# Kernel optimization log

Hardware: AMD Instinct MI355X
Metric: run time of the kernel (lower is better)

The kernel has to match this reference:

```python
import jax, jax.numpy as jnp
import numpy as np

# ---- constants from init_kwargs ----
LAM = 0.05      # lam_l2
CG_MAX = 10     # cg_max
B, C, H, W = 8, 12, 384, 384
EPS = 1e-12


def _cplx(a):
    # [..., 2] real/imag -> complex
    return jax.lax.complex(a[..., 0], a[..., 1])


def _ri(z):
    return jnp.stack([jnp.real(z), jnp.imag(z)], axis=-1)


def setup_inputs() -> dict:
    key = jax.random.key(0)
    k1, k2, k3, k4 = jax.random.split(key, 4)
    x = jax.random.normal(k1, (B, H, W, 2), dtype=jnp.float32)
    adj = jax.random.normal(k2, (B, H, W, 2), dtype=jnp.float32)  # A^H b
    maps = jax.random.normal(k3, (B, C, H, W, 2), dtype=jnp.float32) / np.sqrt(C).astype(np.float32)
    mask = (jax.random.uniform(k4, (B, H, W)) < 0.4).astype(jnp.float32)
    return {"x": x, "adj": adj, "maps": maps, "mask": mask}


def reference(x, adj, maps, mask):
    xc = _cplx(x)          # [B,H,W] complex image (network estimate)
    adjc = _cplx(adj)      # [B,H,W] A^H b
    mc = _cplx(maps)       # [B,C,H,W] coil sensitivities
    maskc = mask.astype(jnp.complex64)[:, None]  # [B,1,H,W]

    def normal(v):
        # SENSE normal operator: A^H A v
        cim = mc * v[:, None]                               # [B,C,H,W]
        k = jnp.fft.fft2(cim, norm="ortho")
        im = jnp.fft.ifft2(k * maskc, norm="ortho")
        return jnp.sum(jnp.conj(mc) * im, axis=1)           # [B,H,W]

    def Aop(v):
        # (A^H A + lam I) v
        return normal(v) + LAM * v

    def zdot(a, b):
        # per-batch real inner product Re<a,b>
        return jnp.real(jnp.sum(jnp.conj(a) * b, axis=(1, 2)))[:, None, None]

    # rhs = adj + lam * x ; CG initialized at rhs (flare.ConjGrad.forward(rhs))
    rhs = adjc + LAM * xc
    x0 = rhs
    r = rhs - Aop(x0)
    p = r
    rd = zdot(r, r)

    def step(carry, _):
        xk, r, p, rd = carry
        Ap = Aop(p)
        alpha = rd / (zdot(p, Ap) + EPS)
        xk = xk + alpha * p
        r = r - alpha * Ap
        rd_new = zdot(r, r)
        beta = rd_new / (rd + EPS)
        p = r + beta * p
        return (xk, r, p, rd_new), None

    (xk, _, _, _), _ = jax.lax.scan(step, (x0, r, p, rd), None, length=CG_MAX)
    return _ri(xk)  # [B,H,W,2]
```

## Files before the change

### kernel.cpp

```cpp
#include <hip/hip_runtime.h>
#include <math.h>

#define BB 8
#define CC 12
#define HH 384
#define WW 384
#define NPIX (HH*WW)
#define LAMF 0.05f
#define EPSF 1e-12f
#define NITER 10

typedef float2 c2;

__device__ __forceinline__ c2 mkc(float x, float y){ c2 r; r.x=x; r.y=y; return r; }
__device__ __forceinline__ c2 cadd(c2 a, c2 b){ return mkc(a.x+b.x, a.y+b.y); }
__device__ __forceinline__ c2 csub(c2 a, c2 b){ return mkc(a.x-b.x, a.y-b.y); }
__device__ __forceinline__ c2 cmul(c2 a, c2 b){ return mkc(a.x*b.x - a.y*b.y, a.x*b.y + a.y*b.x); }
__device__ __forceinline__ c2 cmulcj(c2 a, c2 b){ return mkc(a.x*b.x + a.y*b.y, a.x*b.y - a.y*b.x); }
__device__ __forceinline__ c2 cax(float s, c2 a, c2 b){ return mkc(fmaf(s,a.x,b.x), fmaf(s,a.y,b.y)); }
__device__ __forceinline__ c2 rot90(c2 a, float d){ return mkc(d*a.y, -d*a.x); }

template<int DIR> __device__ __forceinline__ void dft3(c2&a0,c2&a1,c2&a2){
  const float d=(float)DIR;
  c2 t=cadd(a1,a2), s=csub(a1,a2);
  c2 m=mkc(a0.x-0.5f*t.x, a0.y-0.5f*t.y);
  const float c=0.8660254037844386f*d;
  c2 w=mkc(c*s.y, -c*s.x);
  a0=cadd(a0,t); a1=cadd(m,w); a2=csub(m,w);
}
template<int DIR> __device__ __forceinline__ void dft6(c2 u[6]){
  c2 e0=u[0],e1=u[2],e2=u[4], o0=u[1],o1=u[3],o2=u[5];
  dft3<DIR>(e0,e1,e2); dft3<DIR>(o0,o1,o2);
  const float d=(float)DIR, q=0.8660254037844386f*d;
  c2 w1=mkc(0.5f,-q), w2=mkc(-0.5f,-q);
  c2 b1=cmul(w1,o1), b2=cmul(w2,o2);
  u[0]=cadd(e0,o0); u[3]=csub(e0,o0);
  u[1]=cadd(e1,b1); u[4]=csub(e1,b1);
  u[2]=cadd(e2,b2); u[5]=csub(e2,b2);
}
template<int DIR> __device__ __forceinline__ void dft8(c2 u[8]){
  const float d=(float)DIR;
  c2 t0=cadd(u[0],u[4]), t1=csub(u[0],u[4]);
  c2 t2=cadd(u[2],u[6]), t3=csub(u[2],u[6]);
  c2 E0=cadd(t0,t2), E2=csub(t0,t2);
  c2 r3=rot90(t3,d);
  c2 E1=cadd(t1,r3), E3=csub(t1,r3);
  c2 s0=cadd(u[1],u[5]), s1=csub(u[1],u[5]);
  c2 s2=cadd(u[3],u[7]), s3=csub(u[3],u[7]);
  c2 O0=cadd(s0,s2), O2v=csub(s0,s2);
  c2 r7=rot90(s3,d);
  c2 O1=cadd(s1,r7), O3=csub(s1,r7);
  const float rs=0.7071067811865476f;
  c2 w81=mkc(rs,-rs*d), w83=mkc(-rs,-rs*d);
  O1=cmul(w81,O1); O2v=rot90(O2v,d); O3=cmul(w83,O3);
  u[0]=cadd(E0,O0); u[4]=csub(E0,O0);
  u[1]=cadd(E1,O1); u[5]=csub(E1,O1);
  u[2]=cadd(E2,O2v); u[6]=csub(E2,O2v);
  u[3]=cadd(E3,O3); u[7]=csub(E3,O3);
}

__device__ __forceinline__ int pidx(int i){ return i + (i/48); }

__device__ __forceinline__ void make_tw(int t, c2 tw2[7], c2 tw3[7]){
  const float TP = 6.28318530717958647692f;
  int k2 = t % 6;
  #pragma unroll
  for (int j=1;j<8;j++){
    float s,c;
    sincosf(-TP*(float)(k2*j)*(1.0f/48.0f), &s, &c);
    tw2[j-1]=mkc(c,s);
    sincosf(-TP*(float)(t*j)*(1.0f/384.0f), &s, &c);
    tw3[j-1]=mkc(c,s);
  }
}

template<int DIR>
__device__ __forceinline__ void fft384(c2 u6[6], c2 o8[8], c2* SA, c2* SB,
                                       int t, const c2 tw2[7], const c2 tw3[7])
{
  dft6<DIR>(u6);
  #pragma unroll
  for (int j=0;j<6;j++) SA[pidx(6*t+j)] = u6[j];
  __syncthreads();
  if (t<48){
    c2 u[8];
    #pragma unroll
    for (int j=0;j<8;j++) u[j]=SA[pidx(t+48*j)];
    #pragma unroll
    for (int j=1;j<8;j++){
      c2 w=tw2[j-1]; if (DIR<0) w.y=-w.y;
      u[j]=cmul(u[j],w);
    }
    dft8<DIR>(u);
    int k=t%6; int base=(t-k)*8+k;
    #pragma unroll
    for (int j=0;j<8;j++) SB[pidx(base+6*j)]=u[j];
  }
  __syncthreads();
  if (t<48){
    c2 u[8];
    #pragma unroll
    for (int j=0;j<8;j++) u[j]=SB[pidx(t+48*j)];
    #pragma unroll
    for (int j=1;j<8;j++){
      c2 w=tw3[j-1]; if (DIR<0) w.y=-w.y;
      u[j]=cmul(u[j],w);
    }
    dft8<DIR>(u);
    #pragma unroll
    for (int j=0;j<8;j++) o8[j]=u[j];
  }
}

template<int MODE>
__global__ __launch_bounds__(256)
void k1_fwd(const c2* __restrict__ xin, const c2* __restrict__ adj,
            const c2* __restrict__ maps, c2* __restrict__ WK,
            const c2* __restrict__ rbuf, const c2* __restrict__ pin,
            c2* __restrict__ pout, const float* __restrict__ bNum,
            const float* __restrict__ bDen)
{
  __shared__ c2 tile[16][387];
  __shared__ c2 scratch[4][2][392];
  const int tid=threadIdx.x, t=tid&63, wv=tid>>6;
  const int NT=HH/16;
  int bid=blockIdx.x;
  int ht=bid%NT, c=(bid/NT)%CC, b=bid/(NT*CC);
  int h0=ht*16;
  c2 tw2[7], tw3[7]; make_tw(t,tw2,tw3);
  float beta=0.f;
  if (MODE==1) beta = bNum[b]/(bDen[b]+EPSF);
  c2* SA=scratch[wv][0];
  c2* SB=scratch[wv][1];
  const c2* mb = maps + (size_t)(b*CC+c)*NPIX;
  for (int i=0;i<4;i++){
    int rr=wv*4+i, h=h0+rr;
    size_t ro=((size_t)b*HH+h)*WW;
    const c2* mrow=mb+(size_t)h*WW;
    c2 u6[6];
    #pragma unroll
    for (int j=0;j<6;j++){
      int w=t+64*j;
      c2 v;
      if (MODE==0){
        v = cax(LAMF, xin[ro+w], adj[ro+w]);
      } else {
        v = cax(beta, pin[ro+w], rbuf[ro+w]);
        if (c==0) pout[ro+w]=v;
      }
      u6[j]=cmul(mrow[w], v);
    }
    c2 o8[8];
    fft384<1>(u6,o8,SA,SB,t,tw2,tw3);
    if (t<48){
      #pragma unroll
      for (int j=0;j<8;j++) tile[rr][t+48*j]=o8[j];
    }
  }
  __syncthreads();
  c2* wkc = WK + (size_t)(b*CC+c)*NPIX;
  int rl=tid&15, wg=tid>>4;
  for (int it=0;it<24;it++){
    int w=it*16+wg;
    wkc[(size_t)w*HH + h0 + rl] = tile[rl][w];
  }
}

__global__ __launch_bounds__(256)
void k2_mid(c2* __restrict__ WK, const float* __restrict__ maskT)
{
  __shared__ c2 scratch[4][2][392];
  const int tid=threadIdx.x, t=tid&63, wv=tid>>6;
  const int NT=WW/16;
  int bid=blockIdx.x;
  int wt=bid%NT, c=(bid/NT)%CC, b=bid/(NT*CC);
  c2 tw2[7], tw3[7]; make_tw(t,tw2,tw3);
  c2* SA=scratch[wv][0]; c2* SB=scratch[wv][1];
  for (int i=0;i<4;i++){
    int w=wt*16+wv*4+i;
    c2* row = WK + ((size_t)(b*CC+c)*WW + w)*HH;
    const float* mrow = maskT + ((size_t)b*WW + w)*HH;
    c2 u6[6];
    #pragma unroll
    for (int j=0;j<6;j++) u6[j]=row[t+64*j];
    c2 o8[8];
    fft384<1>(u6,o8,SA,SB,t,tw2,tw3);
    __syncthreads();
    if (t<48){
      #pragma unroll
      for (int j=0;j<8;j++){
        float m=mrow[t+48*j];
        c2 v=o8[j];
        SB[t+48*j]=mkc(v.x*m, v.y*m);
      }
    }
    __syncthreads();
    #pragma unroll
    for (int j=0;j<6;j++) u6[j]=SB[t+64*j];
    __syncthreads();
    c2 o8b[8];
    fft384<-1>(u6,o8b,SA,SB,t,tw2,tw3);
    if (t<48){
      #pragma unroll
      for (int j=0;j<8;j++) row[t+48*j]=o8b[j];
    }
  }
}

template<int MODE>
__global__ __launch_bounds__(256)
void k3_inv(const c2* __restrict__ WK, const c2* __restrict__ maps,
            const c2* __restrict__ xin, const c2* __restrict__ adj,
            const c2* __restrict__ pin, c2* __restrict__ rbuf,
            c2* __restrict__ Apbuf, c2* __restrict__ xout,
            float* __restrict__ accslot)
{
  __shared__ c2 tile[8][387];
  __shared__ c2 scratch[4][2][392];
  const int tid=threadIdx.x, t=tid&63, wv=tid>>6;
  const int NT=HH/8;
  int bid=blockIdx.x;
  int ht=bid%NT, b=bid/NT;
  int h0=ht*8;
  c2 tw2[7],tw3[7]; make_tw(t,tw2,tw3);
  c2* SA=scratch[wv][0]; c2* SB=scratch[wv][1];
  c2 acc[2][8];
  #pragma unroll
  for(int a=0;a<2;a++){
    #pragma unroll
    for(int q=0;q<8;q++) acc[a][q]=mkc(0.f,0.f);
  }
  int jj=tid&7, wq=tid>>3;
  for (int c=0;c<CC;c++){
    const c2* wkc = WK + (size_t)(b*CC+c)*NPIX;
    __syncthreads();
    for (int it=0;it<12;it++){
      int w=it*32+wq;
      tile[jj][w]=wkc[(size_t)w*HH + h0 + jj];
    }
    __syncthreads();
    const c2* mb = maps + (size_t)(b*CC+c)*NPIX;
    #pragma unroll
    for (int rl=0;rl<2;rl++){
      int j=wv*2+rl, h=h0+j;
      c2 u6[6];
      #pragma unroll
      for (int q=0;q<6;q++) u6[q]=tile[j][t+64*q];
      c2 o8[8];
      fft384<-1>(u6,o8,SA,SB,t,tw2,tw3);
      if (t<48){
        const c2* mrow=mb+(size_t)h*WW;
        #pragma unroll
        for (int q=0;q<8;q++){
          acc[rl][q]=cadd(acc[rl][q], cmulcj(mrow[t+48*q], o8[q]));
        }
      }
    }
  }
  float partial=0.f;
  #pragma unroll
  for (int rl=0;rl<2;rl++){
    int h=h0+wv*2+rl;
    size_t ro=((size_t)b*HH+h)*WW;
    if (t<48){
      #pragma unroll
      for (int q=0;q<8;q++){
        int w=t+48*q;
        if (MODE==0){
          c2 rhs = cax(LAMF, xin[ro+w], adj[ro+w]);
          c2 Ap = cax(LAMF, rhs, acc[rl][q]);
          c2 rv = csub(rhs, Ap);
          rbuf[ro+w]=rv;
          xout[ro+w]=rhs;
          partial = fmaf(rv.x,rv.x,fmaf(rv.y,rv.y,partial));
        } else {
          c2 pv = pin[ro+w];
          c2 Ap = cax(LAMF, pv, acc[rl][q]);
          Apbuf[ro+w]=Ap;
          partial = fmaf(pv.x,Ap.x,fmaf(pv.y,Ap.y,partial));
        }
      }
    }
  }
  #pragma unroll
  for (int o=32;o>0;o>>=1) partial += __shfl_down(partial,o);
  if (t==0) atomicAdd(&accslot[b], partial);
}

__global__ __launch_bounds__(256)
void k4_upd(c2* __restrict__ x, c2* __restrict__ rbuf,
            const c2* __restrict__ p, const c2* __restrict__ Ap,
            const float* __restrict__ rdPrev, const float* __restrict__ pApk,
            float* __restrict__ rdNew)
{
  const int PERB = NPIX/1024;
  int bid=blockIdx.x;
  int b=bid/PERB, blk=bid%PERB;
  float alpha = rdPrev[b]/(pApk[b]+EPSF);
  size_t base=(size_t)b*NPIX + (size_t)blk*1024 + threadIdx.x;
  float partial=0.f;
  #pragma unroll
  for (int i=0;i<4;i++){
    size_t idx=base + i*256;
    c2 pv=p[idx], apv=Ap[idx], xv=x[idx], rv=rbuf[idx];
    xv = cax(alpha, pv, xv);
    rv = cax(-alpha, apv, rv);
    x[idx]=xv; rbuf[idx]=rv;
    partial = fmaf(rv.x,rv.x,fmaf(rv.y,rv.y,partial));
  }
  #pragma unroll
  for (int o=32;o>0;o>>=1) partial += __shfl_down(partial,o);
  if ((threadIdx.x&63)==0) atomicAdd(&rdNew[b], partial);
}

__global__ void kzero(float* scal){ scal[threadIdx.x]=0.f; }

__global__ __launch_bounds__(256)
void kmask(const float* __restrict__ mask, float* __restrict__ maskT)
{
  __shared__ float tile[32][33];
  int bid=blockIdx.x;
  int wt=bid%12, htl=(bid/12)%12, b=bid/144;
  int h0=htl*32, w0=wt*32;
  int tid=threadIdx.x;
  int wl=tid&31, hl=tid>>5;
  for (int it=0;it<4;it++){
    int h=h0+it*8+hl;
    tile[it*8+hl][wl]=mask[((size_t)b*HH+h)*WW + w0+wl];
  }
  __syncthreads();
  int hl2=tid&31, wl2=tid>>5;
  const float SC = 1.0f/((float)HH*(float)WW);
  for (int it=0;it<4;it++){
    int w=w0+it*8+wl2;
    maskT[((size_t)b*WW+w)*HH + h0+hl2] = SC*tile[hl2][it*8+wl2];
  }
}

extern "C" void kernel_launch(void* const* d_in, const int* in_sizes, int n_in,
                              void* d_out, int out_size, void* d_ws, size_t ws_size,
                              hipStream_t stream)
{
  const c2* xin=(const c2*)d_in[0];
  const c2* adj=(const c2*)d_in[1];
  const c2* maps=(const c2*)d_in[2];
  const float* mask=(const float*)d_in[3];
  c2* xout=(c2*)d_out;
  char* wsp=(char*)d_ws;
  size_t off=0;
  c2* WK=(c2*)(wsp+off);    off += (size_t)BB*CC*NPIX*sizeof(c2);
  float* maskT=(float*)(wsp+off); off += (size_t)BB*NPIX*sizeof(float);
  c2* rbuf=(c2*)(wsp+off);  off += (size_t)BB*NPIX*sizeof(c2);
  c2* pA=(c2*)(wsp+off);    off += (size_t)BB*NPIX*sizeof(c2);
  c2* pB=(c2*)(wsp+off);    off += (size_t)BB*NPIX*sizeof(c2);
  c2* Apb=(c2*)(wsp+off);   off += (size_t)BB*NPIX*sizeof(c2);
  float* scal=(float*)(wsp+off);
  float* rd=scal;
  float* pAp=scal+11*BB;
  float* zslot=scal+22*BB;

  kzero<<<1,256,0,stream>>>(scal);
  kmask<<<BB*144,256,0,stream>>>(mask,maskT);

  k1_fwd<0><<<BB*CC*(HH/16),256,0,stream>>>(xin,adj,maps,WK,rbuf,pA,pB,zslot,zslot);
  k2_mid<<<BB*CC*(WW/16),256,0,stream>>>(WK,maskT);
  k3_inv<0><<<BB*(HH/8),256,0,stream>>>(WK,maps,xin,adj,pA,rbuf,Apb,xout,rd);

  for (int k=1;k<=NITER;k++){
    c2* pouT = (k&1)? pA: pB;
    c2* pinb = (k&1)? pB: pA;
    const float* bN = (k>=2)? rd+(size_t)(k-1)*BB : zslot;
    const float* bD = (k>=2)? rd+(size_t)(k-2)*BB : zslot;
    k1_fwd<1><<<BB*CC*(HH/16),256,0,stream>>>(xin,adj,maps,WK,rbuf,pinb,pouT,bN,bD);
    k2_mid<<<BB*CC*(WW/16),256,0,stream>>>(WK,maskT);
    k3_inv<1><<<BB*(HH/8),256,0,stream>>>(WK,maps,xin,adj,pouT,rbuf,Apb,xout,pAp+(size_t)k*BB);
    k4_upd<<<BB*(NPIX/1024),256,0,stream>>>(xout,rbuf,pouT,Apb,rd+(size_t)(k-1)*BB,pAp+(size_t)k*BB,rd+(size_t)k*BB);
  }
}
```

Baseline: 3.264 ms.

## Replace block barriers with wave-local LDS fences, fast twiddles, smaller k1 tiles

Each FFT row is handled by one 64-lane wavefront using private scratch, so the block-wide __syncthreads inside fft384 and k2_mid become s_waitcnt lgkmcnt(0) fences. This relies on intra-wavefront lockstep execution. Twiddle generation switches from sincosf to the hardware sin/cos builtins taking revolutions, with slightly lower accuracy. k1_fwd now tiles 8 rows instead of 16, which doubles the grid and halves LDS use for more occupancy, at the cost of shorter transpose write runs.

```diff
diff --git a/kernel.cpp b/kernel.cpp
--- a/kernel.cpp
+++ b/kernel.cpp
@@ -19,6 +19,10 @@
 __device__ __forceinline__ c2 cmulcj(c2 a, c2 b){ return mkc(a.x*b.x + a.y*b.y, a.x*b.y - a.y*b.x); }
 __device__ __forceinline__ c2 cax(float s, c2 a, c2 b){ return mkc(fmaf(s,a.x,b.x), fmaf(s,a.y,b.y)); }
 __device__ __forceinline__ c2 rot90(c2 a, float d){ return mkc(d*a.y, -d*a.x); }
+
+__device__ __forceinline__ void lds_fence(){
+  asm volatile("s_waitcnt lgkmcnt(0)" ::: "memory");
+}
 
 template<int DIR> __device__ __forceinline__ void dft3(c2&a0,c2&a1,c2&a2){
   const float d=(float)DIR;
@@ -61,16 +65,17 @@
 
 __device__ __forceinline__ int pidx(int i){ return i + (i/48); }
 
+__device__ __forceinline__ c2 twid(float rev){
+  float r = rev - floorf(rev);
+  return mkc(__builtin_amdgcn_cosf(r), -__builtin_amdgcn_sinf(r));
+}
+
 __device__ __forceinline__ void make_tw(int t, c2 tw2[7], c2 tw3[7]){
-  const float TP = 6.28318530717958647692f;
   int k2 = t % 6;
   #pragma unroll
   for (int j=1;j<8;j++){
-    float s,c;
-    sincosf(-TP*(float)(k2*j)*(1.0f/48.0f), &s, &c);
-    tw2[j-1]=mkc(c,s);
-    sincosf(-TP*(float)(t*j)*(1.0f/384.0f), &s, &c);
-    tw3[j-1]=mkc(c,s);
+    tw2[j-1] = twid((float)(k2*j) * (1.0f/48.0f));
+    tw3[j-1] = twid((float)(t*j)  * (1.0f/384.0f));
   }
 }
 
@@ -81,7 +86,7 @@
   dft6<DIR>(u6);
   #pragma unroll
   for (int j=0;j<6;j++) SA[pidx(6*t+j)] = u6[j];
-  __syncthreads();
+  lds_fence();
   if (t<48){
     c2 u[8];
     #pragma unroll
@@ -95,20 +100,18 @@
     int k=t%6; int base=(t-k)*8+k;
     #pragma unroll
     for (int j=0;j<8;j++) SB[pidx(base+6*j)]=u[j];
-  }
-  __syncthreads();
-  if (t<48){
-    c2 u[8];
-    #pragma unroll
-    for (int j=0;j<8;j++) u[j]=SB[pidx(t+48*j)];
+    lds_fence();
+    c2 v[8];
+    #pragma unroll
+    for (int j=0;j<8;j++) v[j]=SB[pidx(t+48*j)];
     #pragma unroll
     for (int j=1;j<8;j++){
       c2 w=tw3[j-1]; if (DIR<0) w.y=-w.y;
-      u[j]=cmul(u[j],w);
-    }
-    dft8<DIR>(u);
-    #pragma unroll
-    for (int j=0;j<8;j++) o8[j]=u[j];
+      v[j]=cmul(v[j],w);
+    }
+    dft8<DIR>(v);
+    #pragma unroll
+    for (int j=0;j<8;j++) o8[j]=v[j];
   }
 }
 
@@ -120,21 +123,21 @@
             c2* __restrict__ pout, const float* __restrict__ bNum,
             const float* __restrict__ bDen)
 {
-  __shared__ c2 tile[16][387];
+  __shared__ c2 tile[8][387];
   __shared__ c2 scratch[4][2][392];
   const int tid=threadIdx.x, t=tid&63, wv=tid>>6;
-  const int NT=HH/16;
+  const int NT=HH/8;
   int bid=blockIdx.x;
   int ht=bid%NT, c=(bid/NT)%CC, b=bid/(NT*CC);
-  int h0=ht*16;
+  int h0=ht*8;
   c2 tw2[7], tw3[7]; make_tw(t,tw2,tw3);
   float beta=0.f;
   if (MODE==1) beta = bNum[b]/(bDen[b]+EPSF);
   c2* SA=scratch[wv][0];
   c2* SB=scratch[wv][1];
   const c2* mb = maps + (size_t)(b*CC+c)*NPIX;
-  for (int i=0;i<4;i++){
-    int rr=wv*4+i, h=h0+rr;
+  for (int i=0;i<2;i++){
+    int rr=wv*2+i, h=h0+rr;
     size_t ro=((size_t)b*HH+h)*WW;
     const c2* mrow=mb+(size_t)h*WW;
     c2 u6[6];
@@ -159,9 +162,9 @@
   }
   __syncthreads();
   c2* wkc = WK + (size_t)(b*CC+c)*NPIX;
-  int rl=tid&15, wg=tid>>4;
-  for (int it=0;it<24;it++){
-    int w=it*16+wg;
+  int rl=tid&7, wg=tid>>3;
+  for (int it=0;it<12;it++){
+    int w=it*32+wg;
     wkc[(size_t)w*HH + h0 + rl] = tile[rl][w];
   }
 }
@@ -185,7 +188,6 @@
     for (int j=0;j<6;j++) u6[j]=row[t+64*j];
     c2 o8[8];
     fft384<1>(u6,o8,SA,SB,t,tw2,tw3);
-    __syncthreads();
     if (t<48){
       #pragma unroll
       for (int j=0;j<8;j++){
@@ -194,10 +196,9 @@
         SB[t+48*j]=mkc(v.x*m, v.y*m);
       }
     }
-    __syncthreads();
+    lds_fence();
     #pragma unroll
     for (int j=0;j<6;j++) u6[j]=SB[t+64*j];
-    __syncthreads();
     c2 o8b[8];
     fft384<-1>(u6,o8b,SA,SB,t,tw2,tw3);
     if (t<48){
@@ -362,7 +363,7 @@
   kzero<<<1,256,0,stream>>>(scal);
   kmask<<<BB*144,256,0,stream>>>(mask,maskT);
 
-  k1_fwd<0><<<BB*CC*(HH/16),256,0,stream>>>(xin,adj,maps,WK,rbuf,pA,pB,zslot,zslot);
+  k1_fwd<0><<<BB*CC*(HH/8),256,0,stream>>>(xin,adj,maps,WK,rbuf,pA,pB,zslot,zslot);
   k2_mid<<<BB*CC*(WW/16),256,0,stream>>>(WK,maskT);
   k3_inv<0><<<BB*(HH/8),256,0,stream>>>(WK,maps,xin,adj,pA,rbuf,Apb,xout,rd);
 
@@ -371,7 +372,7 @@
     c2* pinb = (k&1)? pB: pA;
     const float* bN = (k>=2)? rd+(size_t)(k-1)*BB : zslot;
     const float* bD = (k>=2)? rd+(size_t)(k-2)*BB : zslot;
-    k1_fwd<1><<<BB*CC*(HH/16),256,0,stream>>>(xin,adj,maps,WK,rbuf,pinb,pouT,bN,bD);
+    k1_fwd<1><<<BB*CC*(HH/8),256,0,stream>>>(xin,adj,maps,WK,rbuf,pinb,pouT,bN,bD);
     k2_mid<<<BB*CC*(WW/16),256,0,stream>>>(WK,maskT);
     k3_inv<1><<<BB*(HH/8),256,0,stream>>>(WK,maps,xin,adj,pouT,rbuf,Apb,xout,pAp+(size_t)k*BB);
     k4_upd<<<BB*(NPIX/1024),256,0,stream>>>(xout,rbuf,pouT,Apb,rd+(size_t)(k-1)*BB,pAp+(size_t)k*BB,rd+(size_t)k*BB);
```

New measurement: 2.858 ms. 1.14x faster.
